# Kernel optimization log

Hardware: AMD Instinct MI355X
Metric: run time of the kernel (lower is better)

Reference implementation:

```python
import jax, jax.numpy as jnp
import numpy as np

GROUPS = 64; SIDE = 8; STEPS = 8
TAU = 1.0; FLOOR = 1e-4; EPS = 1e-4
MU = 1.0; DT = 0.1; GAMMA = 0.1
FLOW_W = 1.0; LOCAL_W = 0.5; KEEP_RATIO = 0.5


def _with_floor(m):
    n = m.shape[-1]
    mask = 1.0 - jnp.eye(n, dtype=m.dtype)
    return jnp.maximum(m * mask, FLOOR * mask)


def _norm_scores(s):
    mean = s.mean(axis=1, keepdims=True)
    std = jnp.clip(s.std(axis=1, ddof=1, keepdims=True), 1e-6, None)  # torch unbiased std
    return (s - mean) / std


def _router_core(tokens, cls_token, W, grid_h, grid_w):
    B, P, D = tokens.shape
    # group ids from patch grid position (patch_indices defaults to arange)
    pi = jnp.broadcast_to(jnp.arange(P), (B, P))
    row, col = pi // grid_w, pi % grid_w
    gh = -(-grid_h // SIDE); gw = -(-grid_w // SIDE)  # ceil div
    gid = jnp.minimum(row // gh, SIDE - 1) * SIDE + jnp.minimum(col // gw, SIDE - 1)  # [B,P]
    # mean-pool tokens per group (scatter_add + count)
    seg = jax.vmap(lambda t, g: jax.ops.segment_sum(t, g, num_segments=GROUPS))
    grouped = seg(tokens, gid)                                 # [B,G,D]
    counts = seg(jnp.ones((B, P, 1), tokens.dtype), gid)       # [B,G,1]
    grouped = grouped / jnp.maximum(counts, 1.0)
    nodes = jnp.concatenate([cls_token[:, None, :], grouped], axis=1)  # [B,G+1,D]
    # pairwise conductance: project, l2-normalize, squared cdist, exp kernel
    proj = jnp.einsum('bnd,ed->bne', nodes, W)  # Linear (no bias): x @ W.T
    proj = proj / jnp.maximum(jnp.linalg.norm(proj, axis=-1, keepdims=True), 1e-12)
    sq = jnp.sum(proj * proj, axis=-1)
    d2 = jnp.maximum(sq[:, :, None] + sq[:, None, :]
                     - 2.0 * jnp.einsum('bnd,bmd->bnm', proj, proj), 0.0)
    C = _with_floor(jnp.exp(-d2 / TAU))
    C = 0.5 * (C + jnp.swapaxes(C, -1, -2))  # symmetric
    # source: cls node injects, groups drain
    source = jnp.full((B, GROUPS + 1), -1.0 / GROUPS, C.dtype).at[:, 0].set(1.0)
    N = GROUPS + 1
    I = jnp.eye(N, dtype=C.dtype)
    d_list, q_list = [C], []
    for _ in range(STEPS):
        deg = C.sum(-1)
        system = deg[:, :, None] * I - C + EPS * I            # Laplacian + eps*I
        p = jnp.linalg.solve(system, source[..., None])[..., 0]
        flow = C * (p[:, :, None] - p[:, None, :])
        q_list.append(flow)
        r = jnp.abs(flow) ** MU
        r = r / (1.0 + r)
        C = C + DT * (r - GAMMA * C)
        C = _with_floor(jnp.maximum(C, 0.0))
        C = _with_floor(0.5 * (C + jnp.swapaxes(C, -1, -2)))
        d_list.append(C)
    return C, jnp.stack(d_list, 1), jnp.stack(q_list, 1), gid


def setup_inputs() -> dict:
    key = jax.random.key(0)
    k1, k2, k3, k4 = jax.random.split(key, 4)
    B, P, D = 64, 576, 768
    return {
        'tokens': jax.random.normal(k1, (B, P, D), jnp.float32),
        'cls_token': jax.random.normal(k2, (B, D), jnp.float32),
        'W': jax.random.normal(k3, (D, D), jnp.float32) / np.sqrt(D),
        'local_scores': jax.random.normal(k4, (B, P), jnp.float32),
        'grid_h': 24,
        'grid_w': 24,
    }


def reference(tokens, cls_token, W, local_scores, grid_h, grid_w):
    B, P, _ = tokens.shape
    final_d, d_hist, q_hist, gid = _router_core(tokens, cls_token, W, grid_h, grid_w)
    routing = final_d[:, 1:, 1:]
    routing = routing / jnp.clip(routing.sum(-1, keepdims=True), 1e-6, None)
    group_flow = jnp.abs(q_hist[:, -1, 1:, :]).sum(-1)        # [B,G]
    group_scores = jnp.take_along_axis(_norm_scores(group_flow), gid, axis=1)
    token_scores = FLOW_W * group_scores + LOCAL_W * _norm_scores(local_scores)
    keep_count = max(1, int(round(P * KEEP_RATIO)))
    _, topk = jax.lax.top_k(token_scores, keep_count)
    patch_keep_mask = jnp.zeros((B, P), bool).at[jnp.arange(B)[:, None], topk].set(True)
    keep_mask = jnp.concatenate([jnp.ones((B, 1), bool), patch_keep_mask], axis=1)
    delta = d_hist[:, 1:] - d_hist[:, :-1]
    aux_sparse = final_d[:, 1:, 1:].sum(axis=(-1, -2)).mean()
    aux_stable = jnp.abs(delta).sum(axis=(-1, -2, -3)).mean()
    return (keep_mask, patch_keep_mask, gid, group_scores, d_hist, q_hist,
            routing, aux_sparse, aux_stable)
```

## Files before the change

### kernel.cpp

```cpp
#include <hip/hip_runtime.h>
#include <stdint.h>

#define NB 64
#define NP 576
#define ND 768
#define NG 64
#define NN 65
#define NSTEPS 8
#define FLOORV 1.0e-4f
#define EPSV   1.0e-4f
#define DTV    0.1f
#define GAMMAV 0.1f
#define KEEPC  288

__global__ __launch_bounds__(256) void k_group_means(const float* __restrict__ tokens,
                                                     const float* __restrict__ cls,
                                                     float* __restrict__ nodes,
                                                     const int* __restrict__ ghp,
                                                     const int* __restrict__ gwp) {
    int bx = blockIdx.x;
    int b = bx / NN, n = bx - b * NN;
    int tid = threadIdx.x;
    float* orow = nodes + (size_t)bx * ND;
    if (n == 0) {
        for (int d = tid; d < ND; d += 256) orow[d] = cls[(size_t)b * ND + d];
        return;
    }
    int grid_h = *ghp, grid_w = *gwp;
    int gh = (grid_h + 7) / 8, gw = (grid_w + 7) / 8;
    int g = n - 1, gr = g >> 3, gc = g & 7;
    int r0 = gr * gh, r1 = (gr == 7) ? grid_h : min((gr + 1) * gh, grid_h);
    int c0 = gc * gw, c1 = (gc == 7) ? grid_w : min((gc + 1) * gw, grid_w);
    int cnt = (r1 > r0 && c1 > c0) ? (r1 - r0) * (c1 - c0) : 0;
    float cf = (float)max(cnt, 1);
    const float* tb = tokens + (size_t)b * NP * ND;
    for (int d = tid; d < ND; d += 256) {
        float acc = 0.f;
        for (int r = r0; r < r1; ++r)
            for (int c = c0; c < c1; ++c)
                acc += tb[(size_t)(r * grid_w + c) * ND + d];
        orow[d] = acc / cf;
    }
}

__global__ __launch_bounds__(256) void k_gemm_nt(const float* __restrict__ A,
                                                 const float* __restrict__ Bm,
                                                 float* __restrict__ Cm) {
    __shared__ float As[32][68];
    __shared__ float Bs[32][68];
    int tid = threadIdx.x;
    int m0 = blockIdx.x * 64, n0 = blockIdx.y * 64;
    int tx = tid & 15, ty = tid >> 4;
    float acc[4][4];
#pragma unroll
    for (int i = 0; i < 4; ++i)
#pragma unroll
        for (int j = 0; j < 4; ++j) acc[i][j] = 0.f;
    int lrow = tid >> 3, lq = tid & 7;
    for (int k0 = 0; k0 < ND; k0 += 32) {
#pragma unroll
        for (int l = 0; l < 2; ++l) {
            int row = lrow + l * 32;
            float4 va = *(const float4*)&A[(size_t)(m0 + row) * ND + k0 + lq * 4];
            As[lq * 4 + 0][row] = va.x; As[lq * 4 + 1][row] = va.y;
            As[lq * 4 + 2][row] = va.z; As[lq * 4 + 3][row] = va.w;
            float4 vb = *(const float4*)&Bm[(size_t)(n0 + row) * ND + k0 + lq * 4];
            Bs[lq * 4 + 0][row] = vb.x; Bs[lq * 4 + 1][row] = vb.y;
            Bs[lq * 4 + 2][row] = vb.z; Bs[lq * 4 + 3][row] = vb.w;
        }
        __syncthreads();
#pragma unroll
        for (int kk = 0; kk < 32; ++kk) {
            float4 a4 = *(const float4*)&As[kk][ty * 4];
            float4 b4 = *(const float4*)&Bs[kk][tx * 4];
            float av[4] = {a4.x, a4.y, a4.z, a4.w};
            float bv[4] = {b4.x, b4.y, b4.z, b4.w};
#pragma unroll
            for (int i = 0; i < 4; ++i)
#pragma unroll
                for (int j = 0; j < 4; ++j) acc[i][j] += av[i] * bv[j];
        }
        __syncthreads();
    }
#pragma unroll
    for (int i = 0; i < 4; ++i) {
        float4 o = make_float4(acc[i][0], acc[i][1], acc[i][2], acc[i][3]);
        *(float4*)&Cm[(size_t)(m0 + ty * 4 + i) * ND + n0 + tx * 4] = o;
    }
}

__global__ __launch_bounds__(256) void k_normalize(float* __restrict__ proj, float* __restrict__ sqv) {
    int r = blockIdx.x, tid = threadIdx.x;
    __shared__ double red[8];
    __shared__ float invs;
    float* row = proj + (size_t)r * ND;
    double s = 0.0;
    for (int d = tid; d < ND; d += 256) { double v = (double)row[d]; s += v * v; }
#pragma unroll
    for (int off = 32; off; off >>= 1) s += __shfl_down(s, off, 64);
    int wid = tid >> 6, lane = tid & 63;
    if (lane == 0) red[wid] = s;
    __syncthreads();
    if (tid == 0) invs = (float)(1.0 / fmax(sqrt(red[0] + red[1] + red[2] + red[3]), 1e-12));
    __syncthreads();
    float inv = invs;
    double s2 = 0.0;
    for (int d = tid; d < ND; d += 256) {
        float v = row[d] * inv; row[d] = v; s2 += (double)v * (double)v;
    }
#pragma unroll
    for (int off = 32; off; off >>= 1) s2 += __shfl_down(s2, off, 64);
    __syncthreads();
    if (lane == 0) red[wid] = s2;
    __syncthreads();
    if (tid == 0) sqv[r] = (float)(red[0] + red[1] + red[2] + red[3]);
}

__global__ __launch_bounds__(256) void k_pairwise(const float* __restrict__ proj,
                                                  const float* __restrict__ sqv,
                                                  float* __restrict__ dhist) {
    int b = blockIdx.x, tid = threadIdx.x;
    int tx = tid & 15, ty = tid >> 4;
    __shared__ float Ps[NN][65];
    float acc[5][5];
#pragma unroll
    for (int a = 0; a < 5; ++a)
#pragma unroll
        for (int c = 0; c < 5; ++c) acc[a][c] = 0.f;
    const float* Pb = proj + (size_t)b * NN * ND;
    for (int k0 = 0; k0 < ND; k0 += 64) {
        __syncthreads();
        for (int idx = tid; idx < NN * 64; idx += 256) {
            int i = idx >> 6, kk = idx & 63;
            Ps[i][kk] = Pb[(size_t)i * ND + k0 + kk];
        }
        __syncthreads();
        for (int kk = 0; kk < 64; ++kk) {
            float av[5], bv[5];
#pragma unroll
            for (int a = 0; a < 5; ++a) { int i = ty + 16 * a; av[a] = (i < NN) ? Ps[i][kk] : 0.f; }
#pragma unroll
            for (int c = 0; c < 5; ++c) { int j = tx + 16 * c; bv[c] = (j < NN) ? Ps[j][kk] : 0.f; }
#pragma unroll
            for (int a = 0; a < 5; ++a)
#pragma unroll
                for (int c = 0; c < 5; ++c) acc[a][c] += av[a] * bv[c];
        }
    }
#pragma unroll
    for (int a = 0; a < 5; ++a)
#pragma unroll
        for (int c = 0; c < 5; ++c) {
            int i = ty + 16 * a, j = tx + 16 * c;
            if (i < NN && j < NN) {
                float d2 = fmaxf(sqv[b * NN + i] + sqv[b * NN + j] - 2.0f * acc[a][c], 0.f);
                double cv = exp(-(double)d2);
                float cf = (i == j) ? 0.f : fmaxf((float)cv, FLOORV);
                dhist[(size_t)b * 9 * NN * NN + (size_t)i * NN + j] = cf;
            }
        }
}

__device__ __forceinline__ float rl(float v, int l) {
    return __int_as_float(__builtin_amdgcn_readlane(__float_as_int(v), l));
}

#define REP64(M) \
  M(1) M(2) M(3) M(4) M(5) M(6) M(7) M(8) M(9) M(10) M(11) M(12) M(13) M(14) M(15) M(16) \
  M(17) M(18) M(19) M(20) M(21) M(22) M(23) M(24) M(25) M(26) M(27) M(28) M(29) M(30) M(31) M(32) \
  M(33) M(34) M(35) M(36) M(37) M(38) M(39) M(40) M(41) M(42) M(43) M(44) M(45) M(46) M(47) M(48) \
  M(49) M(50) M(51) M(52) M(53) M(54) M(55) M(56) M(57) M(58) M(59) M(60) M(61) M(62) M(63) M(64)

#define REP64_2(M, K) \
  M(1,K) M(2,K) M(3,K) M(4,K) M(5,K) M(6,K) M(7,K) M(8,K) M(9,K) M(10,K) M(11,K) M(12,K) \
  M(13,K) M(14,K) M(15,K) M(16,K) M(17,K) M(18,K) M(19,K) M(20,K) M(21,K) M(22,K) M(23,K) M(24,K) \
  M(25,K) M(26,K) M(27,K) M(28,K) M(29,K) M(30,K) M(31,K) M(32,K) M(33,K) M(34,K) M(35,K) M(36,K) \
  M(37,K) M(38,K) M(39,K) M(40,K) M(41,K) M(42,K) M(43,K) M(44,K) M(45,K) M(46,K) M(47,K) M(48,K) \
  M(49,K) M(50,K) M(51,K) M(52,K) M(53,K) M(54,K) M(55,K) M(56,K) M(57,K) M(58,K) M(59,K) M(60,K) \
  M(61,K) M(62,K) M(63,K) M(64,K)

#define LD(J)  float a##J = crow[J];
#define ACCJ(J) deg += a##J;
#define FIXJ(J) a##J = ((J) == i_own) ? diag : -a##J;
#define R0(J)  a##J = __builtin_fmaf(l0, rl(v0, (J) - 1), a##J);
#define UPD(J, K) if ((J) > (K)) a##J = __builtin_fmaf(ln, rl(a##J, (K) - 1), a##J);
#define ROUND(K) { \
    float pk = rl(a##K, (K) - 1); \
    float invp = 1.0f / pk; \
    inv_own = (lane == (K) - 1) ? invp : inv_own; \
    float l = (lane >= (K)) ? a##K * invp : 0.f; \
    float ln = -l; \
    REP64_2(UPD, K) \
    ar = __builtin_fmaf(ln, rl(ar, (K) - 1), ar); \
  }
#define BS(I) { \
    float t = (rhs_ - acc) * inv_own; \
    float pi = rl(t, (I) - 1); \
    p_own = (i_own == (I)) ? t : p_own; \
    acc = __builtin_fmaf((i_own < (I)) ? a##I : 0.f, pi, acc); \
  }

__global__ __launch_bounds__(64, 1) void k_dynamics(float* __restrict__ dhist,
                                                    float* __restrict__ qhist,
                                                    double* __restrict__ part) {
    int b = blockIdx.x;
    int lane = threadIdx.x;
    __shared__ float Cs[NN * NN];
    __shared__ float pd[NN];
    float* C0 = dhist + (size_t)b * 9 * NN * NN;
    for (int t = lane; t < NN * NN; t += 64) Cs[t] = C0[t];
    __threadfence_block();

    const int i_own = lane + 1;
    double stable = 0.0, sparse = 0.0;

#pragma unroll 1
    for (int step = 0; step < NSTEPS; ++step) {
        const float* crow = Cs + (size_t)i_own * NN;
        REP64(LD)
        float c0v = crow[0];
        float deg = c0v;
        REP64(ACCJ)
        float diag = deg + EPSV;
        REP64(FIXJ)
        float ar = -(1.0f / 64.0f);

        float v0 = Cs[lane + 1];
        float s0 = v0;
#pragma unroll
        for (int off = 1; off < 64; off <<= 1) s0 += __shfl_xor(s0, off, 64);
        float d0 = s0 + EPSV;
        float invd0 = 1.0f / d0;
        float l0 = -c0v * invd0;
        REP64(R0)
        ar -= l0;

        float inv_own = 0.f;
        ROUND(1)  ROUND(2)  ROUND(3)  ROUND(4)  ROUND(5)  ROUND(6)  ROUND(7)  ROUND(8)
        ROUND(9)  ROUND(10) ROUND(11) ROUND(12) ROUND(13) ROUND(14) ROUND(15) ROUND(16)
        ROUND(17) ROUND(18) ROUND(19) ROUND(20) ROUND(21) ROUND(22) ROUND(23) ROUND(24)
        ROUND(25) ROUND(26) ROUND(27) ROUND(28) ROUND(29) ROUND(30) ROUND(31) ROUND(32)
        ROUND(33) ROUND(34) ROUND(35) ROUND(36) ROUND(37) ROUND(38) ROUND(39) ROUND(40)
        ROUND(41) ROUND(42) ROUND(43) ROUND(44) ROUND(45) ROUND(46) ROUND(47) ROUND(48)
        ROUND(49) ROUND(50) ROUND(51) ROUND(52) ROUND(53) ROUND(54) ROUND(55) ROUND(56)
        ROUND(57) ROUND(58) ROUND(59) ROUND(60) ROUND(61) ROUND(62) ROUND(63)
        {
            float pk = rl(a64, 63);
            float invp = 1.0f / pk;
            inv_own = (lane == 63) ? invp : inv_own;
        }

        float rhs_ = ar;
        float acc = 0.f, p_own = 0.f;
        BS(64) BS(63) BS(62) BS(61) BS(60) BS(59) BS(58) BS(57)
        BS(56) BS(55) BS(54) BS(53) BS(52) BS(51) BS(50) BS(49)
        BS(48) BS(47) BS(46) BS(45) BS(44) BS(43) BS(42) BS(41)
        BS(40) BS(39) BS(38) BS(37) BS(36) BS(35) BS(34) BS(33)
        BS(32) BS(31) BS(30) BS(29) BS(28) BS(27) BS(26) BS(25)
        BS(24) BS(23) BS(22) BS(21) BS(20) BS(19) BS(18) BS(17)
        BS(16) BS(15) BS(14) BS(13) BS(12) BS(11) BS(10) BS(9)
        BS(8)  BS(7)  BS(6)  BS(5)  BS(4)  BS(3)  BS(2)  BS(1)
        pd[i_own] = p_own;
        float sp = v0 * p_own;
#pragma unroll
        for (int off = 1; off < 64; off <<= 1) sp += __shfl_xor(sp, off, 64);
        if (lane == 0) pd[0] = (1.0f + sp) * invd0;
        __threadfence_block();

        float* qout = qhist + ((size_t)b * NSTEPS + step) * NN * NN;
        float* dout = dhist + ((size_t)b * 9 + step + 1) * NN * NN;
        for (int t = lane; t < NN * NN; t += 64) {
            int i = t / NN, j = t - i * NN;
            float c = Cs[t];
            float fl = c * (pd[i] - pd[j]);
            qout[t] = fl;
            float rr = fabsf(fl); rr = rr / (1.0f + rr);
            float cn = c + DTV * (rr - GAMMAV * c);
            float cnf = (i == j) ? 0.0f : fmaxf(cn, FLOORV);
            Cs[t] = cnf;
            dout[t] = cnf;
            stable += fabs((double)cnf - (double)c);
            if (step == NSTEPS - 1 && i > 0 && j > 0) sparse += (double)cnf;
        }
        __threadfence_block();
    }

#pragma unroll
    for (int off = 32; off; off >>= 1) {
        stable += __shfl_down(stable, off, 64);
        sparse += __shfl_down(sparse, off, 64);
    }
    if (lane == 0) {
        part[b]      = sparse;
        part[NB + b] = stable;
    }
}

__global__ __launch_bounds__(256) void k_scores(const float* __restrict__ qhist,
                                                const float* __restrict__ local,
                                                const int* __restrict__ ghp,
                                                const int* __restrict__ gwp,
                                                float* __restrict__ keep,
                                                float* __restrict__ patch,
                                                float* __restrict__ gidout,
                                                float* __restrict__ gsout) {
    int b = blockIdx.x, tid = threadIdx.x;
    __shared__ double gf[NG];
    __shared__ double ts[NP];
    __shared__ double red[8];
    __shared__ double stats[2];
    if (tid < NG) {
        const float* qrow = qhist + ((size_t)b * NSTEPS + (NSTEPS - 1)) * NN * NN + (size_t)(tid + 1) * NN;
        double s = 0.0;
        for (int j = 0; j < NN; ++j) s += fabs((double)qrow[j]);
        gf[tid] = s;
    }
    __syncthreads();
    if (tid < 64) {
        double v = gf[tid];
        double s = v;
#pragma unroll
        for (int off = 32; off; off >>= 1) s += __shfl_down(s, off, 64);
        double mean = __shfl(s, 0, 64) / (double)NG;
        double d = v - mean, ss = d * d;
#pragma unroll
        for (int off = 32; off; off >>= 1) ss += __shfl_down(ss, off, 64);
        if (tid == 0) { stats[0] = mean; stats[1] = 1.0 / fmax(sqrt(ss / (NG - 1)), 1e-6); }
    }
    const float* lrow = local + (size_t)b * NP;
    double s1 = 0.0;
    for (int p = tid; p < NP; p += 256) s1 += (double)lrow[p];
#pragma unroll
    for (int off = 32; off; off >>= 1) s1 += __shfl_down(s1, off, 64);
    int wid = tid >> 6, lane = tid & 63;
    if (lane == 0) red[wid] = s1;
    __syncthreads();
    double lmean = (red[0] + red[1] + red[2] + red[3]) / (double)NP;
    double s2 = 0.0;
    for (int p = tid; p < NP; p += 256) { double d = (double)lrow[p] - lmean; s2 += d * d; }
#pragma unroll
    for (int off = 32; off; off >>= 1) s2 += __shfl_down(s2, off, 64);
    __syncthreads();
    if (lane == 0) red[wid] = s2;
    __syncthreads();
    double linv = 1.0 / fmax(sqrt((red[0] + red[1] + red[2] + red[3]) / (double)(NP - 1)), 1e-6);
    double gmean = stats[0], ginv = stats[1];
    int grid_h = *ghp, grid_w = *gwp;
    int gh = (grid_h + 7) / 8, gw = (grid_w + 7) / 8;
    for (int p = tid; p < NP; p += 256) {
        int row = p / grid_w, col = p - row * grid_w;
        int g = min(row / gh, 7) * 8 + min(col / gw, 7);
        double gsc = (gf[g] - gmean) * ginv;
        double lsc = ((double)lrow[p] - lmean) * linv;
        ts[p] = gsc + 0.5 * lsc;
        gidout[(size_t)b * NP + p] = (float)g;
        gsout[(size_t)b * NP + p]  = (float)gsc;
    }
    __syncthreads();
    for (int p = tid; p < NP; p += 256) {
        double sp = ts[p];
        int c = 0;
        for (int qq = 0; qq < NP; ++qq) {
            double v = ts[qq];
            c += (v > sp) || (v == sp && qq < p);
        }
        float kf = (c < KEEPC) ? 1.0f : 0.0f;
        patch[(size_t)b * NP + p] = kf;
        keep[(size_t)b * (NP + 1) + 1 + p] = kf;
    }
    if (tid == 0) keep[(size_t)b * (NP + 1)] = 1.0f;
}

__global__ void k_routing(const float* __restrict__ dhist, float* __restrict__ rout) {
    int b = blockIdx.x, tid = threadIdx.x;
    const float* Crow = dhist + ((size_t)b * 9 + 8) * NN * NN + (size_t)(tid + 1) * NN + 1;
    double s = 0.0;
    for (int j = 0; j < NG; ++j) s += (double)Crow[j];
    double inv = 1.0 / fmax(s, 1e-6);
    float* orow = rout + ((size_t)b * NG + tid) * NG;
    for (int j = 0; j < NG; ++j) orow[j] = (float)((double)Crow[j] * inv);
}

__global__ void k_aux(const double* __restrict__ part, float* __restrict__ osp, float* __restrict__ ost) {
    int tid = threadIdx.x;
    double sp = part[tid], st = part[NB + tid];
#pragma unroll
    for (int off = 32; off; off >>= 1) {
        sp += __shfl_down(sp, off, 64);
        st += __shfl_down(st, off, 64);
    }
    if (tid == 0) { *osp = (float)(sp / NB); *ost = (float)(st / NB); }
}

extern "C" void kernel_launch(void* const* d_in, const int* in_sizes, int n_in,
                              void* d_out, int out_size, void* d_ws, size_t ws_size,
                              hipStream_t stream) {
    const float* tokens = (const float*)d_in[0];
    const float* cls    = (const float*)d_in[1];
    const float* W      = (const float*)d_in[2];
    const float* local  = (const float*)d_in[3];
    const int* ghp = (const int*)d_in[4];
    const int* gwp = (const int*)d_in[5];

    float* out = (float*)d_out;
    float* o_keep  = out;
    float* o_patch = o_keep + (size_t)NB * (NP + 1);
    float* o_gid   = o_patch + (size_t)NB * NP;
    float* o_gs    = o_gid + (size_t)NB * NP;
    float* o_dh    = o_gs + (size_t)NB * NP;
    float* o_qh    = o_dh + (size_t)NB * 9 * NN * NN;
    float* o_rt    = o_qh + (size_t)NB * NSTEPS * NN * NN;
    float* o_sp    = o_rt + (size_t)NB * NG * NG;
    float* o_st    = o_sp + 1;

    float* nodes = (float*)d_ws;
    float* proj  = nodes + (size_t)NB * NN * ND;
    float* sqv   = proj + (size_t)NB * NN * ND;
    double* part = (double*)(((uintptr_t)(sqv + NB * NN) + 15) & ~(uintptr_t)15);

    k_group_means<<<NB * NN, 256, 0, stream>>>(tokens, cls, nodes, ghp, gwp);
    dim3 g2((NB * NN) / 64, ND / 64);
    k_gemm_nt<<<g2, 256, 0, stream>>>(nodes, W, proj);
    k_normalize<<<NB * NN, 256, 0, stream>>>(proj, sqv);
    k_pairwise<<<NB, 256, 0, stream>>>(proj, sqv, o_dh);
    k_dynamics<<<NB, 64, 0, stream>>>(o_dh, o_qh, part);
    k_scores<<<NB, 256, 0, stream>>>(o_qh, local, ghp, gwp, o_keep, o_patch, o_gid, o_gs);
    k_routing<<<NB, 64, 0, stream>>>(o_dh, o_rt);
    k_aux<<<1, 64, 0, stream>>>(part, o_sp, o_st);
}
```

Baseline: 709.1 us.

## Split register-resident LU factorization into two column halves to cut VGPR pressure

```diff
diff --git a/kernel.cpp b/kernel.cpp
--- a/kernel.cpp
+++ b/kernel.cpp
@@ -165,39 +165,62 @@
     return __int_as_float(__builtin_amdgcn_readlane(__float_as_int(v), l));
 }
 
-#define REP64(M) \
+#define REP32(M) \
   M(1) M(2) M(3) M(4) M(5) M(6) M(7) M(8) M(9) M(10) M(11) M(12) M(13) M(14) M(15) M(16) \
-  M(17) M(18) M(19) M(20) M(21) M(22) M(23) M(24) M(25) M(26) M(27) M(28) M(29) M(30) M(31) M(32) \
-  M(33) M(34) M(35) M(36) M(37) M(38) M(39) M(40) M(41) M(42) M(43) M(44) M(45) M(46) M(47) M(48) \
-  M(49) M(50) M(51) M(52) M(53) M(54) M(55) M(56) M(57) M(58) M(59) M(60) M(61) M(62) M(63) M(64)
-
-#define REP64_2(M, K) \
+  M(17) M(18) M(19) M(20) M(21) M(22) M(23) M(24) M(25) M(26) M(27) M(28) M(29) M(30) M(31) M(32)
+
+#define REP32_2(M, K) \
   M(1,K) M(2,K) M(3,K) M(4,K) M(5,K) M(6,K) M(7,K) M(8,K) M(9,K) M(10,K) M(11,K) M(12,K) \
   M(13,K) M(14,K) M(15,K) M(16,K) M(17,K) M(18,K) M(19,K) M(20,K) M(21,K) M(22,K) M(23,K) M(24,K) \
-  M(25,K) M(26,K) M(27,K) M(28,K) M(29,K) M(30,K) M(31,K) M(32,K) M(33,K) M(34,K) M(35,K) M(36,K) \
-  M(37,K) M(38,K) M(39,K) M(40,K) M(41,K) M(42,K) M(43,K) M(44,K) M(45,K) M(46,K) M(47,K) M(48,K) \
-  M(49,K) M(50,K) M(51,K) M(52,K) M(53,K) M(54,K) M(55,K) M(56,K) M(57,K) M(58,K) M(59,K) M(60,K) \
-  M(61,K) M(62,K) M(63,K) M(64,K)
-
-#define LD(J)  float a##J = crow[J];
-#define ACCJ(J) deg += a##J;
-#define FIXJ(J) a##J = ((J) == i_own) ? diag : -a##J;
-#define R0(J)  a##J = __builtin_fmaf(l0, rl(v0, (J) - 1), a##J);
-#define UPD(J, K) if ((J) > (K)) a##J = __builtin_fmaf(ln, rl(a##J, (K) - 1), a##J);
-#define ROUND(K) { \
+  M(25,K) M(26,K) M(27,K) M(28,K) M(29,K) M(30,K) M(31,K) M(32,K)
+
+#define LDA(J)   float a##J = crow[J];
+#define ACCA(J)  deg += a##J;
+#define ACCR(J)  deg += crow[32 + (J)];
+#define FIXA(J)  a##J = ((J) == i_own) ? diag : -a##J;
+#define R0A(J)   a##J = __builtin_fmaf(l0, Cs[(J)], a##J);
+#define UPDA(J, K) if ((J) > (K)) a##J = __builtin_fmaf(ln, rl(a##J, (K) - 1), a##J);
+#define ROUNDA(K) { \
     float pk = rl(a##K, (K) - 1); \
     float invp = 1.0f / pk; \
     inv_own = (lane == (K) - 1) ? invp : inv_own; \
     float l = (lane >= (K)) ? a##K * invp : 0.f; \
+    lds_L[(K) * 64 + lane] = l; \
     float ln = -l; \
-    REP64_2(UPD, K) \
+    REP32_2(UPDA, K) \
     ar = __builtin_fmaf(ln, rl(ar, (K) - 1), ar); \
   }
-#define BS(I) { \
+#define DUMPA(J) lds_U[lane * 33 + (J)] = a##J;
+#define LDB(J)   float b##J = ((32 + (J)) == i_own) ? diag : -crow[32 + (J)];
+#define R0B(J)   b##J = __builtin_fmaf(l0, Cs[32 + (J)], b##J);
+#define UPDB(J, K) b##J = __builtin_fmaf(ln, rl(b##J, (K) - 1), b##J);
+#define ROUNDB(K) { \
+    float l = lds_L[(K) * 64 + lane]; \
+    float ln = -l; \
+    REP32_2(UPDB, K) \
+  }
+#define UPDC(J, K) if (((J) + 32) > (K)) b##J = __builtin_fmaf(ln, rl(b##J, (K) - 1), b##J);
+#define ROUNDC(Q, K) { \
+    float pk = rl(b##Q, (K) - 1); \
+    float invp = 1.0f / pk; \
+    inv_own = (lane == (K) - 1) ? invp : inv_own; \
+    float l = (lane >= (K)) ? b##Q * invp : 0.f; \
+    float ln = -l; \
+    REP32_2(UPDC, K) \
+    ar = __builtin_fmaf(ln, rl(ar, (K) - 1), ar); \
+  }
+#define BSH(Q, I) { \
     float t = (rhs_ - acc) * inv_own; \
     float pi = rl(t, (I) - 1); \
     p_own = (i_own == (I)) ? t : p_own; \
-    acc = __builtin_fmaf((i_own < (I)) ? a##I : 0.f, pi, acc); \
+    acc = __builtin_fmaf((i_own < (I)) ? b##Q : 0.f, pi, acc); \
+  }
+#define BSL(I) { \
+    float t = (rhs_ - acc) * inv_own; \
+    float pi = rl(t, (I) - 1); \
+    p_own = (i_own == (I)) ? t : p_own; \
+    float u = lds_U[lane * 33 + (I)]; \
+    acc = __builtin_fmaf((i_own < (I)) ? u : 0.f, pi, acc); \
   }
 
 __global__ __launch_bounds__(64, 1) void k_dynamics(float* __restrict__ dhist,
@@ -207,6 +230,8 @@
     int lane = threadIdx.x;
     __shared__ float Cs[NN * NN];
     __shared__ float pd[NN];
+    __shared__ float lds_L[33 * 64];
+    __shared__ float lds_U[64 * 33];
     float* C0 = dhist + (size_t)b * 9 * NN * NN;
     for (int t = lane; t < NN * NN; t += 64) Cs[t] = C0[t];
     __threadfence_block();
@@ -217,12 +242,13 @@
 #pragma unroll 1
     for (int step = 0; step < NSTEPS; ++step) {
         const float* crow = Cs + (size_t)i_own * NN;
-        REP64(LD)
         float c0v = crow[0];
         float deg = c0v;
-        REP64(ACCJ)
+        REP32(LDA)
+        REP32(ACCA)
+        REP32(ACCR)
         float diag = deg + EPSV;
-        REP64(FIXJ)
+        REP32(FIXA)
         float ar = -(1.0f / 64.0f);
 
         float v0 = Cs[lane + 1];
@@ -232,34 +258,46 @@
         float d0 = s0 + EPSV;
         float invd0 = 1.0f / d0;
         float l0 = -c0v * invd0;
-        REP64(R0)
+        REP32(R0A)
         ar -= l0;
 
         float inv_own = 0.f;
-        ROUND(1)  ROUND(2)  ROUND(3)  ROUND(4)  ROUND(5)  ROUND(6)  ROUND(7)  ROUND(8)
-        ROUND(9)  ROUND(10) ROUND(11) ROUND(12) ROUND(13) ROUND(14) ROUND(15) ROUND(16)
-        ROUND(17) ROUND(18) ROUND(19) ROUND(20) ROUND(21) ROUND(22) ROUND(23) ROUND(24)
-        ROUND(25) ROUND(26) ROUND(27) ROUND(28) ROUND(29) ROUND(30) ROUND(31) ROUND(32)
-        ROUND(33) ROUND(34) ROUND(35) ROUND(36) ROUND(37) ROUND(38) ROUND(39) ROUND(40)
-        ROUND(41) ROUND(42) ROUND(43) ROUND(44) ROUND(45) ROUND(46) ROUND(47) ROUND(48)
-        ROUND(49) ROUND(50) ROUND(51) ROUND(52) ROUND(53) ROUND(54) ROUND(55) ROUND(56)
-        ROUND(57) ROUND(58) ROUND(59) ROUND(60) ROUND(61) ROUND(62) ROUND(63)
+        ROUNDA(1)  ROUNDA(2)  ROUNDA(3)  ROUNDA(4)  ROUNDA(5)  ROUNDA(6)  ROUNDA(7)  ROUNDA(8)
+        ROUNDA(9)  ROUNDA(10) ROUNDA(11) ROUNDA(12) ROUNDA(13) ROUNDA(14) ROUNDA(15) ROUNDA(16)
+        ROUNDA(17) ROUNDA(18) ROUNDA(19) ROUNDA(20) ROUNDA(21) ROUNDA(22) ROUNDA(23) ROUNDA(24)
+        ROUNDA(25) ROUNDA(26) ROUNDA(27) ROUNDA(28) ROUNDA(29) ROUNDA(30) ROUNDA(31) ROUNDA(32)
+
+        REP32(DUMPA)
+        REP32(LDB)
+
+        REP32(R0B)
+        ROUNDB(1)  ROUNDB(2)  ROUNDB(3)  ROUNDB(4)  ROUNDB(5)  ROUNDB(6)  ROUNDB(7)  ROUNDB(8)
+        ROUNDB(9)  ROUNDB(10) ROUNDB(11) ROUNDB(12) ROUNDB(13) ROUNDB(14) ROUNDB(15) ROUNDB(16)
+        ROUNDB(17) ROUNDB(18) ROUNDB(19) ROUNDB(20) ROUNDB(21) ROUNDB(22) ROUNDB(23) ROUNDB(24)
+        ROUNDB(25) ROUNDB(26) ROUNDB(27) ROUNDB(28) ROUNDB(29) ROUNDB(30) ROUNDB(31) ROUNDB(32)
+
+        ROUNDC(1,33)  ROUNDC(2,34)  ROUNDC(3,35)  ROUNDC(4,36)  ROUNDC(5,37)  ROUNDC(6,38)
+        ROUNDC(7,39)  ROUNDC(8,40)  ROUNDC(9,41)  ROUNDC(10,42) ROUNDC(11,43) ROUNDC(12,44)
+        ROUNDC(13,45) ROUNDC(14,46) ROUNDC(15,47) ROUNDC(16,48) ROUNDC(17,49) ROUNDC(18,50)
+        ROUNDC(19,51) ROUNDC(20,52) ROUNDC(21,53) ROUNDC(22,54) ROUNDC(23,55) ROUNDC(24,56)
+        ROUNDC(25,57) ROUNDC(26,58) ROUNDC(27,59) ROUNDC(28,60) ROUNDC(29,61) ROUNDC(30,62)
+        ROUNDC(31,63)
         {
-            float pk = rl(a64, 63);
+            float pk = rl(b32, 63);
             float invp = 1.0f / pk;
             inv_own = (lane == 63) ? invp : inv_own;
         }
 
         float rhs_ = ar;
         float acc = 0.f, p_own = 0.f;
-        BS(64) BS(63) BS(62) BS(61) BS(60) BS(59) BS(58) BS(57)
-        BS(56) BS(55) BS(54) BS(53) BS(52) BS(51) BS(50) BS(49)
-        BS(48) BS(47) BS(46) BS(45) BS(44) BS(43) BS(42) BS(41)
-        BS(40) BS(39) BS(38) BS(37) BS(36) BS(35) BS(34) BS(33)
-        BS(32) BS(31) BS(30) BS(29) BS(28) BS(27) BS(26) BS(25)
-        BS(24) BS(23) BS(22) BS(21) BS(20) BS(19) BS(18) BS(17)
-        BS(16) BS(15) BS(14) BS(13) BS(12) BS(11) BS(10) BS(9)
-        BS(8)  BS(7)  BS(6)  BS(5)  BS(4)  BS(3)  BS(2)  BS(1)
+        BSH(32,64) BSH(31,63) BSH(30,62) BSH(29,61) BSH(28,60) BSH(27,59) BSH(26,58) BSH(25,57)
+        BSH(24,56) BSH(23,55) BSH(22,54) BSH(21,53) BSH(20,52) BSH(19,51) BSH(18,50) BSH(17,49)
+        BSH(16,48) BSH(15,47) BSH(14,46) BSH(13,45) BSH(12,44) BSH(11,43) BSH(10,42) BSH(9,41)
+        BSH(8,40)  BSH(7,39)  BSH(6,38)  BSH(5,37)  BSH(4,36)  BSH(3,35)  BSH(2,34)  BSH(1,33)
+        BSL(32) BSL(31) BSL(30) BSL(29) BSL(28) BSL(27) BSL(26) BSL(25)
+        BSL(24) BSL(23) BSL(22) BSL(21) BSL(20) BSL(19) BSL(18) BSL(17)
+        BSL(16) BSL(15) BSL(14) BSL(13) BSL(12) BSL(11) BSL(10) BSL(9)
+        BSL(8)  BSL(7)  BSL(6)  BSL(5)  BSL(4)  BSL(3)  BSL(2)  BSL(1)
         pd[i_own] = p_own;
         float sp = v0 * p_own;
 #pragma unroll
```

Result: no change. 707.7 us (-0.2%).
